# Optimization experiments

Hardware: AMD Instinct MI355X
Metric: run time of the kernel (lower is better)

## Reference

```python
import jax, jax.numpy as jnp
import numpy as np

EPS = 1e-5
NUM_HEADS = 6


def _dwconv_bn(x5, W, g, b, m, v, stride):
    # x5: [B, C, H, W, D]; depthwise conv3d (groups=C), kernel 3, pad 1, then eval BatchNorm3d,
    # then rearrange 'b c h w d -> b (h w d) c'
    C = x5.shape[1]
    y = jax.lax.conv_general_dilated(
        x5, W, window_strides=(stride, stride, stride), padding=[(1, 1)] * 3,
        feature_group_count=C, dimension_numbers=('NCDHW', 'OIDHW', 'NCDHW'))
    inv = g / jnp.sqrt(v + EPS)
    y = y * inv[None, :, None, None, None] + (b - m * inv)[None, :, None, None, None]
    B, C2, H, Wd, D = y.shape
    return y.transpose(0, 2, 3, 4, 1).reshape(B, H * Wd * D, C2)


def setup_inputs() -> dict:
    key = jax.random.key(0)
    ks = jax.random.split(key, 24)
    B, T, C = 8, 4096, 384
    hh = ww = dd = 16
    s = 0.02
    inp = {
        'x': jax.random.normal(ks[0], (B, T, C), jnp.float32),
        'conv_q_w': jax.random.normal(ks[1], (C, 1, 3, 3, 3), jnp.float32) * 0.1,
        'conv_k_w': jax.random.normal(ks[2], (C, 1, 3, 3, 3), jnp.float32) * 0.1,
        'conv_v_w': jax.random.normal(ks[3], (C, 1, 3, 3, 3), jnp.float32) * 0.1,
        'bn_q_g': jax.random.uniform(ks[4], (C,), jnp.float32, 0.5, 1.5),
        'bn_q_b': jax.random.normal(ks[5], (C,), jnp.float32) * 0.1,
        'bn_q_m': jax.random.normal(ks[6], (C,), jnp.float32) * 0.1,
        'bn_q_v': jax.random.uniform(ks[7], (C,), jnp.float32, 0.5, 1.5),
        'bn_k_g': jax.random.uniform(ks[8], (C,), jnp.float32, 0.5, 1.5),
        'bn_k_b': jax.random.normal(ks[9], (C,), jnp.float32) * 0.1,
        'bn_k_m': jax.random.normal(ks[10], (C,), jnp.float32) * 0.1,
        'bn_k_v': jax.random.uniform(ks[11], (C,), jnp.float32, 0.5, 1.5),
        'bn_v_g': jax.random.uniform(ks[12], (C,), jnp.float32, 0.5, 1.5),
        'bn_v_b': jax.random.normal(ks[13], (C,), jnp.float32) * 0.1,
        'bn_v_m': jax.random.normal(ks[14], (C,), jnp.float32) * 0.1,
        'bn_v_v': jax.random.uniform(ks[15], (C,), jnp.float32, 0.5, 1.5),
        'wq': jax.random.normal(ks[16], (C, C), jnp.float32) * s,
        'wk': jax.random.normal(ks[17], (C, C), jnp.float32) * s,
        'wv': jax.random.normal(ks[18], (C, C), jnp.float32) * s,
        'proj_w': jax.random.normal(ks[19], (C, C), jnp.float32) * s,
        'proj_b': jax.random.normal(ks[20], (C,), jnp.float32) * s,
        'h': hh, 'w': ww, 'd': dd,
    }
    return inp


def reference(x, conv_q_w, conv_k_w, conv_v_w,
              bn_q_g, bn_q_b, bn_q_m, bn_q_v,
              bn_k_g, bn_k_b, bn_k_m, bn_k_v,
              bn_v_g, bn_v_b, bn_v_m, bn_v_v,
              wq, wk, wv, proj_w, proj_b, h, w, d):
    B, T, C = x.shape
    H = NUM_HEADS
    Dh = C // H
    scale = C ** (-0.5)  # dim_out ** -0.5
    x5 = x.reshape(B, h, w, d, C).transpose(0, 4, 1, 2, 3)  # b (h w d) c -> b c h w d
    q = _dwconv_bn(x5, conv_q_w, bn_q_g, bn_q_b, bn_q_m, bn_q_v, 1)   # [B, T, C]
    k = _dwconv_bn(x5, conv_k_w, bn_k_g, bn_k_b, bn_k_m, bn_k_v, 2)   # [B, Tkv, C]
    v = _dwconv_bn(x5, conv_v_w, bn_v_g, bn_v_b, bn_v_m, bn_v_v, 2)   # [B, Tkv, C]

    def to_heads(t, W):  # Linear (no bias) then 'b t (h d) -> b h t d'
        z = t @ W.T
        return z.reshape(B, -1, H, Dh).transpose(0, 2, 1, 3)

    q = to_heads(q, wq)
    k = to_heads(k, wk)
    v = to_heads(v, wv)
    attn = jax.nn.softmax(jnp.einsum('bhld,bhtd->bhlt', q, k) * scale, axis=-1)
    o = jnp.einsum('bhlt,bhtd->bhld', attn, v)
    o = o.transpose(0, 2, 1, 3).reshape(B, -1, C)  # b h t d -> b t (h d)
    return o @ proj_w.T + proj_b
```

## Files before the change

kernel.cpp:

```cpp
#include <hip/hip_runtime.h>
#include <hip/hip_bf16.h>
#include <stdint.h>


typedef _Float16 f16;
typedef _Float16 f16x8 __attribute__((ext_vector_type(8)));
typedef float f32x4 __attribute__((ext_vector_type(4)));
typedef float f32x16 __attribute__((ext_vector_type(16)));
typedef uint32_t u32;
typedef uint32_t u32x4 __attribute__((ext_vector_type(4)));

#define NC 384
#define MFMA16(A_,B_,C_) __builtin_amdgcn_mfma_f32_16x16x32_f16((A_),(B_),(C_),0,0,0)
#define MFMA32(A_,B_,C_) __builtin_amdgcn_mfma_f32_32x32x16_f16((A_),(B_),(C_),0,0,0)

__device__ __forceinline__ void gll16(const void* g, void* l) {
  __builtin_amdgcn_global_load_lds(
      (__attribute__((address_space(1))) void*)g,
      (__attribute__((address_space(3))) void*)l, 16, 0, 0);
}

__device__ __forceinline__ u32 pkf16(float lo, float hi) {
  return __builtin_bit_cast(u32, __builtin_amdgcn_cvt_pkrtz(lo, hi));
}

__global__ __launch_bounds__(256) void cvt_w(
    const float* __restrict__ s0, const float* __restrict__ s1,
    const float* __restrict__ s2, const float* __restrict__ s3,
    f16* __restrict__ d0, f16* __restrict__ d1,
    f16* __restrict__ d2, f16* __restrict__ d3, int n, float scq)
{
  int i = blockIdx.x * 256 + threadIdx.x;
  if (i < n) {
    d0[i] = (f16)(s0[i] * scq);
    d1[i] = (f16)s1[i]; d2[i] = (f16)s2[i]; d3[i] = (f16)s3[i];
  }
}

__global__ __launch_bounds__(384) void cvt_wt(
    const float* __restrict__ wq, const float* __restrict__ wk, const float* __restrict__ wv,
    const float* __restrict__ bqg, const float* __restrict__ bqb,
    const float* __restrict__ bqm, const float* __restrict__ bqv,
    const float* __restrict__ bkg, const float* __restrict__ bkb,
    const float* __restrict__ bkm, const float* __restrict__ bkv,
    const float* __restrict__ bvg, const float* __restrict__ bvb,
    const float* __restrict__ bvm, const float* __restrict__ bvv,
    float* __restrict__ qT, float* __restrict__ kT, float* __restrict__ vT,
    float* __restrict__ betq, float* __restrict__ betk, float* __restrict__ betv)
{
  const int c = threadIdx.x;
  const int t = blockIdx.x;
  const float invq = bqg[c] * rsqrtf(bqv[c] + 1e-5f);
  const float invk = bkg[c] * rsqrtf(bkv[c] + 1e-5f);
  const float invv = bvg[c] * rsqrtf(bvv[c] + 1e-5f);
  qT[t * 384 + c] = wq[c * 27 + t] * invq;
  kT[t * 384 + c] = wk[c * 27 + t] * invk;
  vT[t * 384 + c] = wv[c * 27 + t] * invv;
  if (t == 0) {
    betq[c] = bqb[c] - bqm[c] * invq;
    betk[c] = bkb[c] - bkm[c] * invk;
    betv[c] = bvb[c] - bvm[c] * invv;
  }
}

__global__ __launch_bounds__(128, 3) void conv_fused(
    const float* __restrict__ x,
    const float* __restrict__ wqT, const float* __restrict__ wkT, const float* __restrict__ wvT,
    const float* __restrict__ betq_, const float* __restrict__ betk_,
    const float* __restrict__ betv_,
    f16* __restrict__ qout, f16* __restrict__ kout, f16* __restrict__ vout)
{
  const int tile = blockIdx.x / 3, cthird = blockIdx.x % 3;
  const int c = cthird * 128 + threadIdx.x;
  const int th = tile >> 3, tw = tile & 7;
  const int b = blockIdx.y;
  const int z0 = blockIdx.z * 8;
  const int h0 = th * 2, w0 = tw * 2;

  float wqr[27], wkr[27], wvr[27];
#pragma unroll
  for (int t = 0; t < 27; ++t) {
    wqr[t] = wqT[t * 384 + c];
    wkr[t] = wkT[t * 384 + c];
    wvr[t] = wvT[t * 384 + c];
  }
  const float betq = betq_[c], betk = betk_[c], betv = betv_[c];

  bool hok[4], wok[4];
#pragma unroll
  for (int a = 0; a < 4; ++a) {
    hok[a] = (unsigned)(h0 - 1 + a) < 16u;
    wok[a] = (unsigned)(w0 - 1 + a) < 16u;
  }
  const float* xb = x + (size_t)b * 4096 * NC + c;

  float win[4][4][4];
  auto ldplane = [&](int s, int iz) {
    const bool zok = (unsigned)iz < 16u;
#pragma unroll
    for (int a = 0; a < 4; ++a)
#pragma unroll
      for (int e = 0; e < 4; ++e) {
        float v = 0.f;
        if (zok && hok[a] && wok[e])
          v = xb[(size_t)((h0 - 1 + a) * 256 + (w0 - 1 + e) * 16 + iz) * NC];
        win[s][a][e] = v;
      }
  };
  ldplane(0, z0 - 1);
  ldplane(1, z0);
  ldplane(2, z0 + 1);

#pragma unroll
  for (int zr = 0; zr < 8; ++zr) {
    const int z = z0 + zr;
    ldplane((zr + 3) & 3, z + 2);
    float aq00 = 0.f, aq01 = 0.f, aq10 = 0.f, aq11 = 0.f;
    float ak = 0.f, av = 0.f;
#pragma unroll
    for (int p = 0; p < 3; ++p) {
      const int s = (zr + p) & 3;
#pragma unroll
      for (int a = 0; a < 3; ++a)
#pragma unroll
        for (int e = 0; e < 3; ++e) {
          const float w00 = win[s][a][e],     w01 = win[s][a][e + 1];
          const float w10 = win[s][a + 1][e], w11 = win[s][a + 1][e + 1];
          const float cq = wqr[a * 9 + e * 3 + p];
          aq00 += w00 * cq; aq01 += w01 * cq;
          aq10 += w10 * cq; aq11 += w11 * cq;
          if ((zr & 1) == 0) {
            ak += w00 * wkr[a * 9 + e * 3 + p];
            av += w00 * wvr[a * 9 + e * 3 + p];
          }
        }
    }
    const size_t qb = (size_t)b * 4096;
    qout[(qb + (h0 + 0) * 256 + (w0 + 0) * 16 + z) * NC + c] = (f16)(aq00 + betq);
    qout[(qb + (h0 + 0) * 256 + (w0 + 1) * 16 + z) * NC + c] = (f16)(aq01 + betq);
    qout[(qb + (h0 + 1) * 256 + (w0 + 0) * 16 + z) * NC + c] = (f16)(aq10 + betq);
    qout[(qb + (h0 + 1) * 256 + (w0 + 1) * 16 + z) * NC + c] = (f16)(aq11 + betq);
    if ((zr & 1) == 0) {
      const size_t t = (size_t)b * 512 + (th * 8 + tw) * 8 + (z >> 1);
      kout[t * NC + c] = (f16)(ak + betk);
      vout[t * NC + c] = (f16)(av + betv);
    }
  }
}

template<int MODE>
__global__ __launch_bounds__(256) void gemm_bt(
    const f16* __restrict__ A, const f16* __restrict__ Bw,
    void* __restrict__ Cout, const float* __restrict__ bias)
{
  __shared__ f16 As[128 * 64];
  __shared__ f16 Bs[128 * 64];
  const int tid = threadIdx.x;
  const int w = tid >> 6, lane = tid & 63;
  const int g = lane >> 4, q = lane & 15;
  const int wr = w >> 1, wc = w & 1;
  const size_t brow = (size_t)blockIdx.y * 128;
  const int bcol = blockIdx.x * 128;
  const int srow = lane >> 3;
  const int sbb  = (lane & 7) ^ (srow & 7);
  f32x4 acc[4][4] = {};
  for (int kt = 0; kt < 6; ++kt) {
    const int k0 = kt * 64;
#pragma unroll
    for (int j = 0; j < 4; ++j) {
      const int s = w * 4 + j;
      gll16(A  + (brow + (size_t)(s * 8 + srow)) * NC + k0 + sbb * 8, (char*)As + s * 1024);
      gll16(Bw + (size_t)(bcol + s * 8 + srow) * NC + k0 + sbb * 8, (char*)Bs + s * 1024);
    }
    __syncthreads();
#pragma unroll
    for (int ks = 0; ks < 2; ++ks) {
      f16x8 af[4], bfr[4];
      const int bb = ((g + 4 * ks) ^ (q & 7)) * 16;
#pragma unroll
      for (int m = 0; m < 4; ++m) {
        af[m]  = *(const f16x8*)((const char*)As + (wr * 64 + m * 16 + q) * 128 + bb);
        bfr[m] = *(const f16x8*)((const char*)Bs + (wc * 64 + m * 16 + q) * 128 + bb);
      }
#pragma unroll
      for (int m = 0; m < 4; ++m)
#pragma unroll
        for (int n = 0; n < 4; ++n)
          acc[m][n] = MFMA16(af[m], bfr[n], acc[m][n]);
    }
    __syncthreads();
  }
  float bvals[4];
  if (MODE == 2) {
#pragma unroll
    for (int n = 0; n < 4; ++n) bvals[n] = bias[bcol + wc * 64 + n * 16 + q];
  }
#pragma unroll
  for (int m = 0; m < 4; ++m) {
#pragma unroll
    for (int n = 0; n < 4; ++n) {
#pragma unroll
      for (int r = 0; r < 4; ++r) {
        const size_t row = brow + wr * 64 + m * 16 + 4 * g + r;
        const int col = bcol + wc * 64 + n * 16 + q;
        const float v = acc[m][n][r];
        if (MODE == 0) {
          ((f16*)Cout)[row * NC + col] = (f16)v;
        } else if (MODE == 1) {
          const size_t bi = row >> 9, t = row & 511;
          ((f16*)Cout)[(bi * NC + col) * 512 + t] = (f16)v;
        } else {
          ((float*)Cout)[row * NC + col] = v + bvals[n];
        }
      }
    }
  }
}

__global__ __launch_bounds__(256) void attn(
    const f16* __restrict__ Qp, const f16* __restrict__ Kp,
    const f16* __restrict__ Vt, f16* __restrict__ O)
{
  __shared__ f16 Ks[2][64 * 64];
  __shared__ f16 Vs[2][64 * 64];
  const int tid = threadIdx.x;
  const int w = tid >> 6, lane = tid & 63;
  const int c = lane & 31, h = lane >> 5;
  const int qt = blockIdx.x, hh = blockIdx.y, b = blockIdx.z;
  const size_t qrow = (size_t)b * 4096 + qt * 128 + w * 32 + c;

  f16x8 qf[4];
#pragma unroll
  for (int ks = 0; ks < 4; ++ks)
    qf[ks] = *(const f16x8*)(Qp + qrow * NC + hh * 64 + ks * 16 + 8 * h);

  f32x16 oa0 = {}, oa1 = {};
  float l_run = 0.f;

  const int r0 = tid >> 3, k0b = tid & 7;
  const int r1 = (tid + 256) >> 3, k1b = tid & 7;
  const f16* ks0 = Kp + ((size_t)b * 512 + r0) * NC + hh * 64 + ((k0b ^ (r0 & 7)) * 8);
  const f16* ks1 = Kp + ((size_t)b * 512 + r1) * NC + hh * 64 + ((k1b ^ (r1 & 7)) * 8);
  const f16* vs0 = Vt + ((size_t)b * NC + hh * 64 + r0) * 512 + ((k0b ^ (r0 & 7)) * 8);
  const f16* vs1 = Vt + ((size_t)b * NC + hh * 64 + r1) * 512 + ((k1b ^ (r1 & 7)) * 8);
  gll16(ks0, (char*)&Ks[0][0] + tid * 16);
  gll16(ks1, (char*)&Ks[0][0] + (tid + 256) * 16);
  gll16(vs0, (char*)&Vs[0][0] + tid * 16);
  gll16(vs1, (char*)&Vs[0][0] + (tid + 256) * 16);

  int buf = 0;
  for (int ch = 0; ch < 8; ++ch) {
    __syncthreads();
    if (ch < 7) {
      gll16(ks0 + (size_t)(ch + 1) * 64 * NC, (char*)&Ks[buf ^ 1][0] + tid * 16);
      gll16(ks1 + (size_t)(ch + 1) * 64 * NC, (char*)&Ks[buf ^ 1][0] + (tid + 256) * 16);
      gll16(vs0 + (ch + 1) * 64, (char*)&Vs[buf ^ 1][0] + tid * 16);
      gll16(vs1 + (ch + 1) * 64, (char*)&Vs[buf ^ 1][0] + (tid + 256) * 16);
    }
    const char* kb = (const char*)&Ks[buf][0];
    const char* vb = (const char*)&Vs[buf][0];
#pragma unroll
    for (int half = 0; half < 2; ++half) {
      f32x16 st = {};
#pragma unroll
      for (int ks = 0; ks < 4; ++ks) {
        const int bo = ((2 * ks + h) ^ (c & 7)) * 16;
        const f16x8 kf = *(const f16x8*)(kb + (32 * half + c) * 128 + bo);
        st = MFMA32(kf, qf[ks], st);
      }
      u32 pk[8];
      float ps0 = 0.f, ps1 = 0.f;
#pragma unroll
      for (int t = 0; t < 8; ++t) {
        const float a0 = __builtin_amdgcn_exp2f(st[2 * t]);
        const float a1 = __builtin_amdgcn_exp2f(st[2 * t + 1]);
        ps0 += a0; ps1 += a1;
        pk[t] = pkf16(a0, a1);
      }
      l_run += ps0 + ps1;
#pragma unroll
      for (int ss = 0; ss < 2; ++ss) {
        const int s = half * 2 + ss, tb = ss * 4;
        const u32 xs = h ? pk[tb + 0] : pk[tb + 2];
        const u32 ys = h ? pk[tb + 1] : pk[tb + 3];
        const u32 rx = __shfl_xor(xs, 32);
        const u32 ry = __shfl_xor(ys, 32);
        u32x4 fi;
        fi[0] = h ? rx : pk[tb + 0];
        fi[1] = h ? ry : pk[tb + 1];
        fi[2] = h ? pk[tb + 2] : rx;
        fi[3] = h ? pk[tb + 3] : ry;
        const f16x8 pfrag = __builtin_bit_cast(f16x8, fi);
        const int bo = ((2 * s + h) ^ (c & 7)) * 16;
        const f16x8 v0 = *(const f16x8*)(vb + c * 128 + bo);
        const f16x8 v1 = *(const f16x8*)(vb + (32 + c) * 128 + bo);
        oa0 = MFMA32(v0, pfrag, oa0);
        oa1 = MFMA32(v1, pfrag, oa1);
      }
    }
    buf ^= 1;
  }
  const float ltot = l_run + __shfl_xor(l_run, 32);
  const float linv = 1.0f / ltot;
  f16* orow = O + qrow * NC + hh * 64;
#pragma unroll
  for (int dt = 0; dt < 2; ++dt) {
#pragma unroll
    for (int qd = 0; qd < 4; ++qd) {
      const float v0 = (dt ? oa1[4 * qd + 0] : oa0[4 * qd + 0]) * linv;
      const float v1 = (dt ? oa1[4 * qd + 1] : oa0[4 * qd + 1]) * linv;
      const float v2 = (dt ? oa1[4 * qd + 2] : oa0[4 * qd + 2]) * linv;
      const float v3 = (dt ? oa1[4 * qd + 3] : oa0[4 * qd + 3]) * linv;
      uint2 pr; pr.x = pkf16(v0, v1); pr.y = pkf16(v2, v3);
      *(uint2*)(orow + dt * 32 + 8 * qd + 4 * h) = pr;
    }
  }
}

extern "C" void kernel_launch(void* const* d_in, const int* in_sizes, int n_in,
                              void* d_out, int out_size, void* d_ws, size_t ws_size,
                              hipStream_t stream) {
  const float* x   = (const float*)d_in[0];
  const float* cqw = (const float*)d_in[1];
  const float* ckw = (const float*)d_in[2];
  const float* cvw = (const float*)d_in[3];
  const float* bqg = (const float*)d_in[4],  *bqb = (const float*)d_in[5];
  const float* bqm = (const float*)d_in[6],  *bqv = (const float*)d_in[7];
  const float* bkg = (const float*)d_in[8],  *bkb = (const float*)d_in[9];
  const float* bkm = (const float*)d_in[10], *bkv = (const float*)d_in[11];
  const float* bvg = (const float*)d_in[12], *bvb = (const float*)d_in[13];
  const float* bvm = (const float*)d_in[14], *bvv = (const float*)d_in[15];
  const float* wq = (const float*)d_in[16];
  const float* wk = (const float*)d_in[17];
  const float* wv = (const float*)d_in[18];
  const float* pw = (const float*)d_in[19];
  const float* pb = (const float*)d_in[20];

  f16* q_tok = (f16*)d_out;
  f16* Qp    = (f16*)((char*)d_out + 25165824);

  char* ws = (char*)d_ws;
  f16* wq_h  = (f16*)(ws + 0);
  f16* wk_h  = (f16*)(ws + 294912);
  f16* wv_h  = (f16*)(ws + 589824);
  f16* pw_h  = (f16*)(ws + 884736);
  f16* k_tok = (f16*)(ws + 1179648);
  f16* v_tok = (f16*)(ws + 4325376);
  f16* Kp    = (f16*)(ws + 7471104);
  f16* Vt    = (f16*)(ws + 10616832);
  f16* Oi    = (f16*)(ws + 13762560);
  float* wqT = (float*)(ws + 38928384);
  float* wkT = (float*)(ws + 38969856);
  float* wvT = (float*)(ws + 39011328);
  float* betq = (float*)(ws + 39052800);
  float* betk = (float*)(ws + 39054336);
  float* betv = (float*)(ws + 39055872);

  const float scq = 0.051031036307982884f * 1.4426950408889634f;
  cvt_w<<<dim3(576), dim3(256), 0, stream>>>(wq, wk, wv, pw, wq_h, wk_h, wv_h, pw_h,
                                             147456, scq);
  cvt_wt<<<dim3(27), dim3(384), 0, stream>>>(
      cqw, ckw, cvw,
      bqg, bqb, bqm, bqv, bkg, bkb, bkm, bkv, bvg, bvb, bvm, bvv,
      wqT, wkT, wvT, betq, betk, betv);
  conv_fused<<<dim3(192, 8, 2), dim3(128), 0, stream>>>(
      x, wqT, wkT, wvT, betq, betk, betv, q_tok, k_tok, v_tok);
  gemm_bt<0><<<dim3(3, 256), dim3(256), 0, stream>>>(q_tok, wq_h, Qp, nullptr);
  gemm_bt<0><<<dim3(3, 32),  dim3(256), 0, stream>>>(k_tok, wk_h, Kp, nullptr);
  gemm_bt<1><<<dim3(3, 32),  dim3(256), 0, stream>>>(v_tok, wv_h, Vt, nullptr);
  attn<<<dim3(32, 6, 8), dim3(256), 0, stream>>>(Qp, Kp, Vt, Oi);
  gemm_bt<2><<<dim3(3, 256), dim3(256), 0, stream>>>(Oi, pw_h, d_out, pb);
}
```

Baseline: 146.1 us.

## Split depthwise conv into one block per z-plane instead of sliding window

The fused depthwise conv kernel now gives each block a single z plane instead of eight, launching 16 z-blocks rather than 2. The sliding 4-plane register window is dropped: each block loads a 3x4x4 neighbourhood and only the q weights into registers. The k/v weights are read from global memory inside the even-z branch. This raises parallelism and lowers register pressure, but gives up the z-direction reuse of input planes, so each input element is loaded about three times more often.

Result: slower. 167.5 us (+14.6%).

```diff
diff --git a/kernel.cpp b/kernel.cpp
--- a/kernel.cpp
+++ b/kernel.cpp
@@ -63,7 +63,7 @@
   }
 }
 
-__global__ __launch_bounds__(128, 3) void conv_fused(
+__global__ __launch_bounds__(128) void conv_z1(
     const float* __restrict__ x,
     const float* __restrict__ wqT, const float* __restrict__ wkT, const float* __restrict__ wvT,
     const float* __restrict__ betq_, const float* __restrict__ betk_,
@@ -74,17 +74,8 @@
   const int c = cthird * 128 + threadIdx.x;
   const int th = tile >> 3, tw = tile & 7;
   const int b = blockIdx.y;
-  const int z0 = blockIdx.z * 8;
+  const int z = blockIdx.z;
   const int h0 = th * 2, w0 = tw * 2;
-
-  float wqr[27], wkr[27], wvr[27];
-#pragma unroll
-  for (int t = 0; t < 27; ++t) {
-    wqr[t] = wqT[t * 384 + c];
-    wkr[t] = wkT[t * 384 + c];
-    wvr[t] = wvT[t * 384 + c];
-  }
-  const float betq = betq_[c], betk = betk_[c], betv = betv_[c];
 
   bool hok[4], wok[4];
 #pragma unroll
@@ -94,8 +85,10 @@
   }
   const float* xb = x + (size_t)b * 4096 * NC + c;
 
-  float win[4][4][4];
-  auto ldplane = [&](int s, int iz) {
+  float win[3][4][4];
+#pragma unroll
+  for (int p = 0; p < 3; ++p) {
+    const int iz = z - 1 + p;
     const bool zok = (unsigned)iz < 16u;
 #pragma unroll
     for (int a = 0; a < 4; ++a)
@@ -104,47 +97,45 @@
         float v = 0.f;
         if (zok && hok[a] && wok[e])
           v = xb[(size_t)((h0 - 1 + a) * 256 + (w0 - 1 + e) * 16 + iz) * NC];
-        win[s][a][e] = v;
-      }
-  };
-  ldplane(0, z0 - 1);
-  ldplane(1, z0);
-  ldplane(2, z0 + 1);
-
-#pragma unroll
-  for (int zr = 0; zr < 8; ++zr) {
-    const int z = z0 + zr;
-    ldplane((zr + 3) & 3, z + 2);
-    float aq00 = 0.f, aq01 = 0.f, aq10 = 0.f, aq11 = 0.f;
+        win[p][a][e] = v;
+      }
+  }
+
+  float wqr[27];
+#pragma unroll
+  for (int t = 0; t < 27; ++t) wqr[t] = wqT[t * 384 + c];
+  float aq00 = 0.f, aq01 = 0.f, aq10 = 0.f, aq11 = 0.f;
+#pragma unroll
+  for (int p = 0; p < 3; ++p)
+#pragma unroll
+    for (int a = 0; a < 3; ++a)
+#pragma unroll
+      for (int e = 0; e < 3; ++e) {
+        const float cq = wqr[a * 9 + e * 3 + p];
+        aq00 += win[p][a][e]         * cq;
+        aq01 += win[p][a][e + 1]     * cq;
+        aq10 += win[p][a + 1][e]     * cq;
+        aq11 += win[p][a + 1][e + 1] * cq;
+      }
+  const float betq = betq_[c];
+  const size_t qb = (size_t)b * 4096;
+  qout[(qb + (h0 + 0) * 256 + (w0 + 0) * 16 + z) * NC + c] = (f16)(aq00 + betq);
+  qout[(qb + (h0 + 0) * 256 + (w0 + 1) * 16 + z) * NC + c] = (f16)(aq01 + betq);
+  qout[(qb + (h0 + 1) * 256 + (w0 + 0) * 16 + z) * NC + c] = (f16)(aq10 + betq);
+  qout[(qb + (h0 + 1) * 256 + (w0 + 1) * 16 + z) * NC + c] = (f16)(aq11 + betq);
+
+  if ((z & 1) == 0) {
     float ak = 0.f, av = 0.f;
 #pragma unroll
-    for (int p = 0; p < 3; ++p) {
-      const int s = (zr + p) & 3;
-#pragma unroll
-      for (int a = 0; a < 3; ++a)
-#pragma unroll
-        for (int e = 0; e < 3; ++e) {
-          const float w00 = win[s][a][e],     w01 = win[s][a][e + 1];
-          const float w10 = win[s][a + 1][e], w11 = win[s][a + 1][e + 1];
-          const float cq = wqr[a * 9 + e * 3 + p];
-          aq00 += w00 * cq; aq01 += w01 * cq;
-          aq10 += w10 * cq; aq11 += w11 * cq;
-          if ((zr & 1) == 0) {
-            ak += w00 * wkr[a * 9 + e * 3 + p];
-            av += w00 * wvr[a * 9 + e * 3 + p];
-          }
-        }
-    }
-    const size_t qb = (size_t)b * 4096;
-    qout[(qb + (h0 + 0) * 256 + (w0 + 0) * 16 + z) * NC + c] = (f16)(aq00 + betq);
-    qout[(qb + (h0 + 0) * 256 + (w0 + 1) * 16 + z) * NC + c] = (f16)(aq01 + betq);
-    qout[(qb + (h0 + 1) * 256 + (w0 + 0) * 16 + z) * NC + c] = (f16)(aq10 + betq);
-    qout[(qb + (h0 + 1) * 256 + (w0 + 1) * 16 + z) * NC + c] = (f16)(aq11 + betq);
-    if ((zr & 1) == 0) {
-      const size_t t = (size_t)b * 512 + (th * 8 + tw) * 8 + (z >> 1);
-      kout[t * NC + c] = (f16)(ak + betk);
-      vout[t * NC + c] = (f16)(av + betv);
-    }
+    for (int t = 0; t < 27; ++t) {
+      const int p = t % 3, e = (t / 3) % 3, a = t / 9;
+      const float wv_ = win[p][a][e];
+      ak += wv_ * wkT[t * 384 + c];
+      av += wv_ * wvT[t * 384 + c];
+    }
+    const size_t t = (size_t)b * 512 + tile * 8 + (z >> 1);
+    kout[t * NC + c] = (f16)(ak + betk_[c]);
+    vout[t * NC + c] = (f16)(av + betv_[c]);
   }
 }
 
@@ -363,7 +354,7 @@
       cqw, ckw, cvw,
       bqg, bqb, bqm, bqv, bkg, bkb, bkm, bkv, bvg, bvb, bvm, bvv,
       wqT, wkT, wvT, betq, betk, betv);
-  conv_fused<<<dim3(192, 8, 2), dim3(128), 0, stream>>>(
+  conv_z1<<<dim3(192, 8, 16), dim3(128), 0, stream>>>(
       x, wqT, wkT, wvT, betq, betk, betv, q_tok, k_tok, v_tok);
   gemm_bt<0><<<dim3(3, 256), dim3(256), 0, stream>>>(q_tok, wq_h, Qp, nullptr);
   gemm_bt<0><<<dim3(3, 32),  dim3(256), 0, stream>>>(k_tok, wk_h, Kp, nullptr);
```
